# Optimization experiments

Hardware: AMD Instinct MI355X
Metric: run time of the kernel (lower is better)

Reference implementation:

```python
import jax, jax.numpy as jnp
import numpy as np
from jax import lax

N, C_IN, C_OUT, H, W = 8, 64, 64, 128, 128
K, KS, STRIDE, PAD, GROUPS = 4, 3, 1, 1, 1


def setup_inputs() -> dict:
    key = jax.random.key(0)
    ks = jax.random.split(key, 10)
    s = 0.05
    return {
        "x": jax.random.normal(ks[0], (N, C_IN, H, W), jnp.float32),
        "weight": jax.random.normal(ks[1], (K, C_OUT, C_IN // GROUPS, KS, KS), jnp.float32) * s,
        "conv_w": jax.random.normal(ks[2], (C_OUT, C_IN, KS, KS), jnp.float32) * s,
        "conv_b": jax.random.normal(ks[3], (C_OUT,), jnp.float32) * s,
        "net0_w": jax.random.normal(ks[4], (K, 1, 1, 1, 1), jnp.float32) * s,
        "net0_b": jax.random.normal(ks[5], (K,), jnp.float32) * s,
        "net1_w": jax.random.normal(ks[6], (K, 1, 3, 3, 3), jnp.float32) * s,
        "net1_b": jax.random.normal(ks[7], (K,), jnp.float32) * s,
        "net2_w": jax.random.normal(ks[8], (K, 1, 5, 3, 3), jnp.float32) * s,
        "net2_b": jax.random.normal(ks[9], (K,), jnp.float32) * s,
    }


def _conv3d_mean(x5, w, b, pad):
    # x5: (N,1,C,H,W); w: (K,1,kd,kh,kw); 'same'-style padding per kernel.
    y = lax.conv_general_dilated(x5, w, (1, 1, 1), [(p, p) for p in pad],
                                 dimension_numbers=('NCDHW', 'OIDHW', 'NCDHW'))
    # global avg pool over (C,H,W); bias is constant so add after the mean.
    return jnp.mean(y, axis=(2, 3, 4)) + b[None, :]


def reference(x, weight, conv_w, conv_b, net0_w, net0_b, net1_w, net1_b, net2_w, net2_b):
    dn2 = ('NCHW', 'OIHW', 'NCHW')
    # static residual conv branch
    r = lax.conv_general_dilated(x, conv_w, (STRIDE, STRIDE), [(PAD, PAD)] * 2,
                                 dimension_numbers=dn2) + conv_b[None, :, None, None]
    # attention over 3D convs of x.unsqueeze(1)
    x5 = x[:, None]  # (N,1,C,H,W)
    logits = (_conv3d_mean(x5, net0_w, net0_b, (0, 0, 0))
              + _conv3d_mean(x5, net1_w, net1_b, (1, 1, 1))
              + _conv3d_mean(x5, net2_w, net2_b, (2, 1, 1)))  # (N,K)
    att = jax.nn.softmax(logits, axis=-1)
    # per-sample dynamic kernel mixing: (N,K) @ (K,out,in/g,kh,kw)
    agg_w = jnp.einsum('nk,koihw->noihw', att, weight)
    # grouped conv with groups = GROUPS*N == per-sample conv (vmapped)
    def per_sample(xi, wi):
        return lax.conv_general_dilated(xi[None], wi, (STRIDE, STRIDE), [(PAD, PAD)] * 2,
                                        dimension_numbers=dn2,
                                        feature_group_count=GROUPS)[0]
    out = jax.vmap(per_sample)(x, agg_w)  # (N,out,H,W)
    return out + r
```

## Files before the change

### kernel.cpp

```cpp
#include <hip/hip_runtime.h>


typedef unsigned short ushort_t;
typedef __attribute__((ext_vector_type(8))) short bf16x8;
typedef __attribute__((ext_vector_type(4))) float f32x4;

__device__ __forceinline__ ushort_t f2bf(float f) {
    unsigned u = __float_as_uint(f);
    unsigned r = (u + 0x7fffu + ((u >> 16) & 1u)) >> 16;
    return (ushort_t)r;
}

__global__ __launch_bounds__(256) void kTR(const float* __restrict__ x,
                                           ushort_t* __restrict__ xt,
                                           float* __restrict__ part) {
    int row = blockIdx.x;
    int h = row & 127, n = row >> 7;
    int tid = threadIdx.x;
    int wg = tid & 31;
    int ci8 = tid >> 5;

    __shared__ float catloc[15];
    if (tid < 15) catloc[tid] = 0.f;
    __syncthreads();

    const float* xp = x + (size_t)(n * 64 + ci8 * 8) * 16384 + h * 128 + wg;
    float v[8][4];
#pragma unroll
    for (int j = 0; j < 8; ++j)
#pragma unroll
        for (int c = 0; c < 4; ++c)
            v[j][c] = xp[j * 16384 + c * 32];

    ushort_t* op = xt + ((size_t)(row * 8 + ci8)) * 128 * 8;
#pragma unroll
    for (int c = 0; c < 4; ++c) {
        ushort_t u[8];
#pragma unroll
        for (int j = 0; j < 8; ++j) u[j] = f2bf(v[j][c]);
        uint4 pk;
        pk.x = (unsigned)u[0] | ((unsigned)u[1] << 16);
        pk.y = (unsigned)u[2] | ((unsigned)u[3] << 16);
        pk.z = (unsigned)u[4] | ((unsigned)u[5] << 16);
        pk.w = (unsigned)u[6] | ((unsigned)u[7] << 16);
        *(uint4*)(op + (size_t)(wg + c * 32) * 8) = pk;
    }

#pragma unroll
    for (int j = 0; j < 8; ++j) {
        float rs = v[j][0] + v[j][1] + v[j][2] + v[j][3];
#pragma unroll
        for (int m = 1; m <= 16; m <<= 1) rs += __shfl_xor(rs, m);
        int ci = ci8 * 8 + j;
        int cd = (ci == 0) ? 0 : (ci == 1) ? 1 : (ci == 62) ? 3 : (ci == 63) ? 4 : 2;
        if (wg == 0) {
            atomicAdd(&catloc[cd * 3 + 0], rs);
            atomicAdd(&catloc[cd * 3 + 1], v[j][0]);
        }
        if (wg == 31) atomicAdd(&catloc[cd * 3 + 2], v[j][3]);
    }
    __syncthreads();
    if (tid < 15) part[row * 16 + tid] = catloc[tid];
}

__global__ __launch_bounds__(256) void kW(const float* __restrict__ part,
                                          const float* __restrict__ nw0, const float* __restrict__ nb0,
                                          const float* __restrict__ nw1, const float* __restrict__ nb1,
                                          const float* __restrict__ nw2, const float* __restrict__ nb2,
                                          const float* __restrict__ weight,
                                          const float* __restrict__ convw,
                                          ushort_t* __restrict__ weff) {
    int bid = blockIdx.x;
    int s = bid % 9;
    int n = bid / 9;
    int tid = threadIdx.x;

    __shared__ float cat_s[45];
    __shared__ float box_s[45];
    __shared__ float tot_s;
    __shared__ float att_s[4];

    if (tid < 45) cat_s[tid] = 0.f;
    __syncthreads();
    if (tid < 128) {
        int h = tid;
        int ch = (h == 0) ? 0 : (h == 127) ? 2 : 1;
        const float* pp = part + (size_t)(n * 128 + h) * 16;
#pragma unroll
        for (int q = 0; q < 15; ++q) {
            int cd = q / 3, st = q % 3;
            atomicAdd(&cat_s[(cd * 3 + ch) * 3 + st], pp[q]);
        }
    }
    __syncthreads();

    if (tid < 46) {
        float c[5][3][3];
#pragma unroll
        for (int i = 0; i < 5; ++i)
#pragma unroll
            for (int j = 0; j < 3; ++j)
#pragma unroll
                for (int t = 0; t < 3; ++t)
                    c[i][j][t] = cat_s[(i * 3 + j) * 3 + t];

        if (tid < 45) {
            int dz = tid / 9 - 2;
            int dy = (tid / 3) % 3 - 1;
            int dx = tid % 3 - 1;
            float acc = 0.f;
#pragma unroll
            for (int cd = 0; cd < 5; ++cd) {
                int dv = (cd == 0) ? 0 : (cd == 1) ? 1 : (cd == 3) ? 62 : (cd == 4) ? 63 : -1;
                bool incd = (dv < 0) || (dv >= dz && dv < 64 + dz);
#pragma unroll
                for (int ch = 0; ch < 3; ++ch) {
                    int hv = (ch == 0) ? 0 : (ch == 2) ? 127 : -1;
                    bool inch = (hv < 0) || (hv >= dy && hv < 128 + dy);
                    if (incd && inch) {
                        float v = c[cd][ch][0];
                        if (dx == -1) v -= c[cd][ch][2];
                        else if (dx == 1) v -= c[cd][ch][1];
                        acc += v;
                    }
                }
            }
            box_s[tid] = acc;
        } else {
            float tot = 0.f;
#pragma unroll
            for (int i = 0; i < 5; ++i)
#pragma unroll
                for (int j = 0; j < 3; ++j) tot += c[i][j][0];
            tot_s = tot;
        }
    }
    __syncthreads();

    if (tid < 4) {
        int k = tid;
        const float invV = 1.0f / (64.f * 128.f * 128.f);
        float lg = nb0[k] + nb1[k] + nb2[k] + nw0[k] * tot_s * invV;
#pragma unroll
        for (int dz = 0; dz < 3; ++dz)
#pragma unroll
            for (int dy = 0; dy < 3; ++dy)
#pragma unroll
                for (int dx = 0; dx < 3; ++dx)
                    lg += nw1[k * 27 + dz * 9 + dy * 3 + dx] *
                          box_s[(dz + 1) * 9 + dy * 3 + dx] * invV;
#pragma unroll
        for (int b = 0; b < 45; ++b)
            lg += nw2[k * 45 + b] * box_s[b] * invV;

        float m = fmaxf(lg, __shfl_xor(lg, 1));
        m = fmaxf(m, __shfl_xor(m, 2));
        float e = __expf(lg - m);
        float ssum = e + __shfl_xor(e, 1);
        ssum += __shfl_xor(ssum, 2);
        att_s[k] = e / ssum;
    }
    __syncthreads();

    float a0 = att_s[0], a1 = att_s[1], a2 = att_s[2], a3 = att_s[3];
    int ci = tid & 63;
    int cog = tid >> 6;
    ushort_t* wp = weff + ((size_t)(n * 9 + s) * 64) * 64;
#pragma unroll
    for (int p = 0; p < 16; ++p) {
        int co = cog * 16 + p;
        size_t base = (size_t)(co * 64 + ci) * 9 + s;
        float v = convw[base]
                + a0 * weight[base]
                + a1 * weight[base +     64 * 64 * 9]
                + a2 * weight[base + 2 * 64 * 64 * 9]
                + a3 * weight[base + 3 * 64 * 64 * 9];
        wp[(size_t)co * 64 + ci] = f2bf(v);
    }
}

__global__ __launch_bounds__(256, 2) void kC(const ushort_t* __restrict__ xt,
                                             const ushort_t* __restrict__ weff,
                                             const float* __restrict__ convb,
                                             float* __restrict__ out) {
    int bid = blockIdx.x;
    int wt = bid & 1;
    int hq = (bid >> 1) & 31;
    int n = bid >> 6;
    int h0 = hq * 4;
    int w0 = wt * 64;

    __shared__ __align__(16) ushort_t lds[6 * 8 * 66 * 8];

    int tid = threadIdx.x;
    int lane = tid & 63;
    int wave = tid >> 6;
    int kq = lane >> 4;
    int l15 = lane & 15;

    for (int idx = tid; idx < 3168; idx += 256) {
        int c = idx % 66;
        int rc8 = idx / 66;
        int r = rc8 >> 3, ci8 = rc8 & 7;
        int hg = h0 + r - 1;
        int wg = w0 + c - 1;
        uint4 vv = make_uint4(0u, 0u, 0u, 0u);
        if (hg >= 0 && hg < 128 && wg >= 0 && wg < 128)
            vv = *(const uint4*)(xt + ((size_t)((n * 128 + hg) * 8 + ci8) * 128 + wg) * 8);
        *(uint4*)&lds[(size_t)idx * 8] = vv;
    }

    int co_a = wave * 16 + l15;
    bf16x8 afrag[9][2];
#pragma unroll
    for (int s = 0; s < 9; ++s)
#pragma unroll
        for (int kc = 0; kc < 2; ++kc)
            afrag[s][kc] = *(const bf16x8*)(weff +
                ((size_t)((n * 9 + s) * 64 + co_a)) * 64 + kc * 32 + kq * 8);

    f32x4 acc[16];
#pragma unroll
    for (int t = 0; t < 16; ++t) acc[t] = (f32x4){0.f, 0.f, 0.f, 0.f};

    __syncthreads();

#pragma unroll
    for (int kx = 0; kx < 3; ++kx) {
#pragma unroll
        for (int kc = 0; kc < 2; ++kc) {
#pragma unroll
            for (int col = 0; col < 4; ++col) {
                bf16x8 brow[6];
#pragma unroll
                for (int p = 0; p < 6; ++p)
                    brow[p] = *(const bf16x8*)
                        &lds[(((p * 8 + kc * 4 + kq) * 66) + col * 16 + l15 + kx) * 8];
#pragma unroll
                for (int ky = 0; ky < 3; ++ky)
#pragma unroll
                    for (int r = 0; r < 4; ++r)
                        acc[r * 4 + col] = __builtin_amdgcn_mfma_f32_16x16x32_bf16(
                            afrag[ky * 3 + kx][kc], brow[r + ky], acc[r * 4 + col], 0, 0, 0);
            }
        }
    }

#pragma unroll
    for (int r = 0; r < 4; ++r) {
        int h = h0 + r;
#pragma unroll
        for (int col = 0; col < 4; ++col) {
            int w = w0 + col * 16 + l15;
#pragma unroll
            for (int reg = 0; reg < 4; ++reg) {
                int co = wave * 16 + kq * 4 + reg;
                float v = acc[r * 4 + col][reg] + convb[co];
                out[(((size_t)n * 64 + co) * 128 + h) * 128 + w] = v;
            }
        }
    }
}

extern "C" void kernel_launch(void* const* d_in, const int* in_sizes, int n_in,
                              void* d_out, int out_size, void* d_ws, size_t ws_size,
                              hipStream_t stream) {
    const float* x      = (const float*)d_in[0];
    const float* weight = (const float*)d_in[1];
    const float* conv_w = (const float*)d_in[2];
    const float* conv_b = (const float*)d_in[3];
    const float* n0w    = (const float*)d_in[4];
    const float* n0b    = (const float*)d_in[5];
    const float* n1w    = (const float*)d_in[6];
    const float* n1b    = (const float*)d_in[7];
    const float* n2w    = (const float*)d_in[8];
    const float* n2b    = (const float*)d_in[9];
    float* out = (float*)d_out;

    char* ws = (char*)d_ws;
    ushort_t* xt   = (ushort_t*)(ws);
    ushort_t* weff = (ushort_t*)(ws + 16777216);
    float*    part = (float*)(ws + 16777216 + 589824);

    kTR<<<1024, 256, 0, stream>>>(x, xt, part);
    kW<<<72, 256, 0, stream>>>(part, n0w, n0b, n1w, n1b, n2w, n2b,
                               weight, conv_w, weff);
    kC<<<512, 256, 0, stream>>>(xt, weff, conv_b, out);
}
```

Before: 131.9 us.

## Fuse bf16 transpose into conv kernel; reduce first kernel to statistics only

The first kernel no longer writes a channel-packed bf16 copy of x. It now only reads x with float4 loads to compute the channel-edge sums needed for attention. The conv kernel loads fp32 x directly, converts it to bf16, and packs it into LDS in an 81-wide padded layout, with a 7-column offset in the fragment reads. This removes a 16 MB write plus its reread, but each conv block now reads fp32 halo tiles (twice the bytes) and does the conversion itself. The halo is 8-aligned, so it is partly wasted.

Result: slower. 135.2 us (+2.5%).

```diff
diff --git a/kernel.cpp b/kernel.cpp
--- a/kernel.cpp
+++ b/kernel.cpp
@@ -11,9 +11,8 @@
     return (ushort_t)r;
 }
 
-__global__ __launch_bounds__(256) void kTR(const float* __restrict__ x,
-                                           ushort_t* __restrict__ xt,
-                                           float* __restrict__ part) {
+__global__ __launch_bounds__(256) void kR(const float* __restrict__ x,
+                                          float* __restrict__ part) {
     int row = blockIdx.x;
     int h = row & 127, n = row >> 7;
     int tid = threadIdx.x;
@@ -24,40 +23,20 @@
     if (tid < 15) catloc[tid] = 0.f;
     __syncthreads();
 
-    const float* xp = x + (size_t)(n * 64 + ci8 * 8) * 16384 + h * 128 + wg;
-    float v[8][4];
-#pragma unroll
-    for (int j = 0; j < 8; ++j)
-#pragma unroll
-        for (int c = 0; c < 4; ++c)
-            v[j][c] = xp[j * 16384 + c * 32];
-
-    ushort_t* op = xt + ((size_t)(row * 8 + ci8)) * 128 * 8;
-#pragma unroll
-    for (int c = 0; c < 4; ++c) {
-        ushort_t u[8];
-#pragma unroll
-        for (int j = 0; j < 8; ++j) u[j] = f2bf(v[j][c]);
-        uint4 pk;
-        pk.x = (unsigned)u[0] | ((unsigned)u[1] << 16);
-        pk.y = (unsigned)u[2] | ((unsigned)u[3] << 16);
-        pk.z = (unsigned)u[4] | ((unsigned)u[5] << 16);
-        pk.w = (unsigned)u[6] | ((unsigned)u[7] << 16);
-        *(uint4*)(op + (size_t)(wg + c * 32) * 8) = pk;
-    }
-
+    const float* xp = x + (size_t)(n * 64 + ci8 * 8) * 16384 + h * 128 + wg * 4;
 #pragma unroll
     for (int j = 0; j < 8; ++j) {
-        float rs = v[j][0] + v[j][1] + v[j][2] + v[j][3];
+        float4 v = *(const float4*)(xp + (size_t)j * 16384);
+        float rs = v.x + v.y + v.z + v.w;
 #pragma unroll
         for (int m = 1; m <= 16; m <<= 1) rs += __shfl_xor(rs, m);
         int ci = ci8 * 8 + j;
         int cd = (ci == 0) ? 0 : (ci == 1) ? 1 : (ci == 62) ? 3 : (ci == 63) ? 4 : 2;
         if (wg == 0) {
             atomicAdd(&catloc[cd * 3 + 0], rs);
-            atomicAdd(&catloc[cd * 3 + 1], v[j][0]);
-        }
-        if (wg == 31) atomicAdd(&catloc[cd * 3 + 2], v[j][3]);
+            atomicAdd(&catloc[cd * 3 + 1], v.x);
+        }
+        if (wg == 31) atomicAdd(&catloc[cd * 3 + 2], v.w);
     }
     __syncthreads();
     if (tid < 15) part[row * 16 + tid] = catloc[tid];
@@ -179,18 +158,18 @@
     }
 }
 
-__global__ __launch_bounds__(256, 2) void kC(const ushort_t* __restrict__ xt,
+__global__ __launch_bounds__(256, 2) void kC(const float* __restrict__ x,
                                              const ushort_t* __restrict__ weff,
                                              const float* __restrict__ convb,
                                              float* __restrict__ out) {
     int bid = blockIdx.x;
-    int wt = bid & 1;
+    int whalf = bid & 1;
     int hq = (bid >> 1) & 31;
     int n = bid >> 6;
     int h0 = hq * 4;
-    int w0 = wt * 64;
-
-    __shared__ __align__(16) ushort_t lds[6 * 8 * 66 * 8];
+    int w0 = whalf * 64;
+
+    __shared__ __align__(16) ushort_t lds[6 * 8 * 81 * 8];
 
     int tid = threadIdx.x;
     int lane = tid & 63;
@@ -198,16 +177,39 @@
     int kq = lane >> 4;
     int l15 = lane & 15;
 
-    for (int idx = tid; idx < 3168; idx += 256) {
-        int c = idx % 66;
-        int rc8 = idx / 66;
-        int r = rc8 >> 3, ci8 = rc8 & 7;
+    for (int t = tid; t < 480; t += 256) {
+        int ci8 = t & 7;
+        int rwt = t >> 3;
+        int wt = rwt % 10;
+        int r = rwt / 10;
         int hg = h0 + r - 1;
-        int wg = w0 + c - 1;
-        uint4 vv = make_uint4(0u, 0u, 0u, 0u);
-        if (hg >= 0 && hg < 128 && wg >= 0 && wg < 128)
-            vv = *(const uint4*)(xt + ((size_t)((n * 128 + hg) * 8 + ci8) * 128 + wg) * 8);
-        *(uint4*)&lds[(size_t)idx * 8] = vv;
+        int wg0 = w0 - 8 + wt * 8;
+        float f[8][8];
+        if (hg >= 0 && hg < 128 && wg0 >= 0 && wg0 <= 120) {
+            const float* xp = x + ((size_t)(n * 64 + ci8 * 8) * 128 + hg) * 128 + wg0;
+#pragma unroll
+            for (int j = 0; j < 8; ++j) {
+                float4 a = *(const float4*)(xp + (size_t)j * 16384);
+                float4 b = *(const float4*)(xp + (size_t)j * 16384 + 4);
+                f[j][0] = a.x; f[j][1] = a.y; f[j][2] = a.z; f[j][3] = a.w;
+                f[j][4] = b.x; f[j][5] = b.y; f[j][6] = b.z; f[j][7] = b.w;
+            }
+        } else {
+#pragma unroll
+            for (int j = 0; j < 8; ++j)
+#pragma unroll
+                for (int e = 0; e < 8; ++e) f[j][e] = 0.f;
+        }
+        ushort_t* dst = &lds[(((size_t)r * 8 + ci8) * 81 + wt * 8) * 8];
+#pragma unroll
+        for (int e = 0; e < 8; ++e) {
+            uint4 pk;
+            pk.x = (unsigned)f2bf(f[0][e]) | ((unsigned)f2bf(f[1][e]) << 16);
+            pk.y = (unsigned)f2bf(f[2][e]) | ((unsigned)f2bf(f[3][e]) << 16);
+            pk.z = (unsigned)f2bf(f[4][e]) | ((unsigned)f2bf(f[5][e]) << 16);
+            pk.w = (unsigned)f2bf(f[6][e]) | ((unsigned)f2bf(f[7][e]) << 16);
+            *(uint4*)(dst + e * 8) = pk;
+        }
     }
 
     int co_a = wave * 16 + l15;
@@ -235,7 +237,8 @@
 #pragma unroll
                 for (int p = 0; p < 6; ++p)
                     brow[p] = *(const bf16x8*)
-                        &lds[(((p * 8 + kc * 4 + kq) * 66) + col * 16 + l15 + kx) * 8];
+                        &lds[(((size_t)p * 8 + kc * 4 + kq) * 81 +
+                              col * 16 + l15 + kx + 7) * 8];
 #pragma unroll
                 for (int ky = 0; ky < 3; ++ky)
 #pragma unroll
@@ -278,12 +281,11 @@
     float* out = (float*)d_out;
 
     char* ws = (char*)d_ws;
-    ushort_t* xt   = (ushort_t*)(ws);
-    ushort_t* weff = (ushort_t*)(ws + 16777216);
-    float*    part = (float*)(ws + 16777216 + 589824);
-
-    kTR<<<1024, 256, 0, stream>>>(x, xt, part);
+    ushort_t* weff = (ushort_t*)(ws);
+    float*    part = (float*)(ws + 589824);
+
+    kR<<<1024, 256, 0, stream>>>(x, part);
     kW<<<72, 256, 0, stream>>>(part, n0w, n0b, n1w, n1b, n2w, n2b,
                                weight, conv_w, weff);
-    kC<<<512, 256, 0, stream>>>(xt, weff, conv_b, out);
-}
+    kC<<<512, 256, 0, stream>>>(x, weff, conv_b, out);
+}
```
